# Optimization experiments

Hardware: AMD Instinct MI355X
Metric: run time of the kernel (lower is better)

Reference implementation:

```python
import jax, jax.numpy as jnp
import numpy as np

NUM_EMBEDDINGS = 1024
EMBEDDING_DIM = 256
COMMITMENT_COST = 0.25


def setup_inputs() -> dict:
    key = jax.random.key(0)
    k1, k2 = jax.random.split(key)
    inputs = jax.random.normal(k1, (64, 256, 32, 32), dtype=jnp.float32)
    # nn.Embedding weight init: uniform(-1/K, 1/K)
    embedding = jax.random.uniform(
        k2, (NUM_EMBEDDINGS, EMBEDDING_DIM), dtype=jnp.float32,
        minval=-1.0 / NUM_EMBEDDINGS, maxval=1.0 / NUM_EMBEDDINGS)
    return {"inputs": inputs, "embedding": embedding}


def reference(inputs, embedding):
    # NCHW -> NHWC, flatten to [N, D]
    x = jnp.transpose(inputs, (0, 2, 3, 1))  # [B,H,W,D]
    input_shape = x.shape
    flat = x.reshape(-1, EMBEDDING_DIM)  # [N, D]

    # squared euclidean distances to all codebook entries: [N, K]
    distances = (jnp.sum(flat ** 2, axis=1, keepdims=True)
                 + jnp.sum(embedding ** 2, axis=1)
                 - 2.0 * flat @ embedding.T)
    idx = jnp.argmin(distances, axis=1)  # [N]

    # one-hot encodings (returned output); quantization via gather is
    # mathematically identical to encodings @ embedding
    encodings = jax.nn.one_hot(idx, NUM_EMBEDDINGS, dtype=embedding.dtype)  # [N,K]
    quantized_flat = embedding[idx]  # [N, D]
    quantized = quantized_flat.reshape(input_shape)  # [B,H,W,D]

    e_latent_loss = jnp.mean((jax.lax.stop_gradient(quantized) - x) ** 2)
    q_latent_loss = jnp.mean((quantized - jax.lax.stop_gradient(x)) ** 2)
    loss = q_latent_loss + COMMITMENT_COST * e_latent_loss

    # straight-through estimator
    quantized_st = x + jax.lax.stop_gradient(quantized - x)

    avg_probs = jnp.mean(encodings, axis=0)  # [K]
    perplexity = jnp.exp(-jnp.sum(avg_probs * jnp.log(avg_probs + 1e-10)))

    quantized_out = jnp.transpose(quantized_st, (0, 3, 1, 2))  # NHWC -> NCHW
    return (loss, quantized_out, perplexity, encodings, quantized_flat)
```

## Files before the change

### kernel.cpp

```cpp
#include <hip/hip_runtime.h>
#include <hip/hip_bf16.h>
#include <math.h>

#define NB    64
#define D     256
#define K     1024
#define HW    1024
#define NTOT  65536
#define MARGIN 1e-5f

#define OUT_QOUT   1
#define OUT_PERP   16777217
#define OUT_ENC    16777218
#define OUT_QFLAT  83886082


typedef __attribute__((ext_vector_type(8))) short bf16x8;
typedef __attribute__((ext_vector_type(4))) float f32x4;

__global__ void enorm_kernel(const float* __restrict__ emb, float* __restrict__ enorm) {
    int k = blockIdx.x * 256 + threadIdx.x;
    const float4* row = (const float4*)(emb + (size_t)k * D);
    float s = 0.f;
    #pragma unroll
    for (int q = 0; q < D / 4; q++) {
        float4 v = row[q];
        s += v.x * v.x + v.y * v.y + v.z * v.z + v.w * v.w;
    }
    enorm[k] = s;
}

__global__ void esplit_kernel(const float* __restrict__ emb, ushort* __restrict__ efrag) {
    const int ntg = blockIdx.x;
    const int t = threadIdx.x;
    __shared__ float sEm[16 * 260];

    {
        const int row = t >> 4, seg = t & 15;
        const float4* src = (const float4*)(emb + (size_t)(ntg * 16 + row) * D + seg * 16);
        float4* dst = (float4*)(sEm + row * 260 + seg * 16);
        #pragma unroll
        for (int q = 0; q < 4; q++) dst[q] = src[q];
    }
    __syncthreads();

    const int w = t >> 6, lane = t & 63;
    for (int fb = w; fb < 16; fb += 4) {
        const int h = fb >> 3, dc = fb & 7;
        const float* srcp = sEm + (lane & 15) * 260 + dc * 32 + (lane >> 4) * 8;
        ushort o[8];
        #pragma unroll
        for (int j = 0; j < 8; j++) {
            float x = srcp[j];
            __hip_bfloat16 hb = __float2bfloat16(x);
            if (h == 0) { o[j] = *(ushort*)&hb; }
            else {
                float hf = __bfloat162float(hb);
                __hip_bfloat16 lb = __float2bfloat16(x - hf);
                o[j] = *(ushort*)&lb;
            }
        }
        ushort* dst = efrag + ((size_t)(h * 64 + ntg) * 8 + dc) * 512 + lane * 8;
        *(int4*)dst = *(int4*)o;
    }
}

__global__ void __attribute__((amdgpu_flat_work_group_size(256, 256), amdgpu_waves_per_eu(2, 2)))
score_mfma_kernel(
    const float* __restrict__ in, const ushort* __restrict__ efrag,
    const float* __restrict__ enorm, int* __restrict__ idx,
    int* __restrict__ rcount, int* __restrict__ rlist)
{
    __shared__ ushort sA[16384];

    const int t = threadIdx.x;
    const int n0 = blockIdx.x * 32;
    const int b = n0 >> 10, p0 = n0 & 1023;
    const int w = t >> 6, lane = t & 63;

    {
        #pragma unroll
        for (int i = 0; i < 4; i++) {
            const int fb = w * 4 + i;
            const int mt = fb >> 3, dc = fb & 7;
            const int m  = mt * 16 + (lane & 15);
            const int d0 = dc * 32 + (lane >> 4) * 8;
            const float* src = in + (size_t)b * (D * HW) + (size_t)d0 * HW + p0 + m;
            ushort oh[8], ol[8];
            #pragma unroll
            for (int j = 0; j < 8; j++) {
                const float x = src[(size_t)j * HW];
                __hip_bfloat16 hb = __float2bfloat16(x);
                const float hf = __bfloat162float(hb);
                __hip_bfloat16 lb = __float2bfloat16(x - hf);
                oh[j] = *(ushort*)&hb;
                ol[j] = *(ushort*)&lb;
            }
            ushort* dh = sA + ((0 * 2 + mt) * 8 + dc) * 512 + lane * 8;
            ushort* dl = sA + ((1 * 2 + mt) * 8 + dc) * 512 + lane * 8;
            *(int4*)dh = *(int4*)oh;
            *(int4*)dl = *(int4*)ol;
        }
    }
    __syncthreads();

    float rm1[8], rm2[8]; int ri[8];
    #pragma unroll
    for (int q = 0; q < 8; q++) { rm1[q] = 3.4e38f; rm2[q] = 3.4e38f; ri[q] = 0; }

    const ushort* efragLo = efrag + 262144;

    for (int kp = 0; kp < 4; kp++) {
        f32x4 acc[2][4];
        #pragma unroll
        for (int mt = 0; mt < 2; mt++)
            #pragma unroll
            for (int c = 0; c < 4; c++) acc[mt][c] = (f32x4){0.f, 0.f, 0.f, 0.f};

        bf16x8 Bh[4][2], Bl[4][2];
        #pragma unroll
        for (int s = 0; s < 3; s++) {
            const int dc = s >> 1, cp = s & 1;
            const int ntg0 = kp * 16 + w * 4 + cp * 2;
            const size_t o0 = ((size_t)(ntg0 * 8 + dc)) * 512 + lane * 8;
            Bh[s][0] = *(const bf16x8*)(efrag + o0);
            Bl[s][0] = *(const bf16x8*)(efragLo + o0);
            Bh[s][1] = *(const bf16x8*)(efrag + o0 + 8 * 512);
            Bl[s][1] = *(const bf16x8*)(efragLo + o0 + 8 * 512);
        }

        bf16x8 ah[2], al[2];
        #pragma unroll
        for (int s = 0; s < 16; s++) {
            const int dc = s >> 1, cp = s & 1;
            if (s + 3 < 16) {
                const int s2 = s + 3, dc2 = s2 >> 1, cp2 = s2 & 1, bs2 = s2 & 3;
                const int ntg0 = kp * 16 + w * 4 + cp2 * 2;
                const size_t o0 = ((size_t)(ntg0 * 8 + dc2)) * 512 + lane * 8;
                Bh[bs2][0] = *(const bf16x8*)(efrag + o0);
                Bl[bs2][0] = *(const bf16x8*)(efragLo + o0);
                Bh[bs2][1] = *(const bf16x8*)(efrag + o0 + 8 * 512);
                Bl[bs2][1] = *(const bf16x8*)(efragLo + o0 + 8 * 512);
            }
            if (cp == 0) {
                #pragma unroll
                for (int mt = 0; mt < 2; mt++) {
                    ah[mt] = *(const bf16x8*)(sA + ((0 * 2 + mt) * 8 + dc) * 512 + lane * 8);
                    al[mt] = *(const bf16x8*)(sA + ((1 * 2 + mt) * 8 + dc) * 512 + lane * 8);
                }
            }
            const int bs = s & 3;
            #pragma unroll
            for (int mt = 0; mt < 2; mt++) {
                #pragma unroll
                for (int cc = 0; cc < 2; cc++) {
                    const int c = cp * 2 + cc;
                    acc[mt][c] = __builtin_amdgcn_mfma_f32_16x16x32_bf16(al[mt], Bh[bs][cc], acc[mt][c], 0, 0, 0);
                    acc[mt][c] = __builtin_amdgcn_mfma_f32_16x16x32_bf16(ah[mt], Bh[bs][cc], acc[mt][c], 0, 0, 0);
                    acc[mt][c] = __builtin_amdgcn_mfma_f32_16x16x32_bf16(ah[mt], Bl[bs][cc], acc[mt][c], 0, 0, 0);
                }
            }
        }

        #pragma unroll
        for (int c = 0; c < 4; c++) {
            const int kcc = kp * 256 + (w * 4 + c) * 16 + (lane & 15);
            const float envc = enorm[kcc];
            #pragma unroll
            for (int mt = 0; mt < 2; mt++)
                #pragma unroll
                for (int r = 0; r < 4; r++) {
                    const int q = mt * 4 + r;
                    const float s = envc - 2.0f * acc[mt][c][r];
                    if (s < rm1[q]) { rm2[q] = rm1[q]; rm1[q] = s; ri[q] = kcc; }
                    else if (s < rm2[q]) rm2[q] = s;
                }
        }
    }

    float f1 = 3.4e38f, f2 = 3.4e38f; int fi = 0;
    #pragma unroll
    for (int q = 0; q < 8; q++) {
        float m1 = rm1[q], m2 = rm2[q]; int i1 = ri[q];
        #pragma unroll
        for (int mask = 1; mask <= 8; mask <<= 1) {
            float o1 = __shfl_xor(m1, mask, 64);
            int   oi = __shfl_xor(i1, mask, 64);
            float o2 = __shfl_xor(m2, mask, 64);
            float n2 = fminf(fminf(m2, o2), fmaxf(m1, o1));
            if (o1 < m1 || (o1 == m1 && oi < i1)) { m1 = o1; i1 = oi; }
            m2 = n2;
        }
        if ((lane & 15) == q) { f1 = m1; f2 = m2; fi = i1; }
    }

    __syncthreads();
    float* sM1 = (float*)sA;
    float* sM2 = sM1 + 128;
    int*   sI  = (int*)(sM2 + 128);
    if ((lane & 15) < 8) {
        const int q = lane & 15;
        const int row = (q >> 2) * 16 + (lane >> 4) * 4 + (q & 3);
        sM1[w * 32 + row] = f1;
        sM2[w * 32 + row] = f2;
        sI [w * 32 + row] = fi;
    }
    __syncthreads();
    if (t < 32) {
        float b1 = sM1[t], b2 = sM2[t]; int bi = sI[t];
        #pragma unroll
        for (int ww = 1; ww < 4; ww++) {
            float a1 = sM1[ww * 32 + t], a2 = sM2[ww * 32 + t]; int ai = sI[ww * 32 + t];
            float n2 = fminf(fminf(b2, a2), fmaxf(b1, a1));
            if (a1 < b1 || (a1 == b1 && ai < bi)) { b1 = a1; bi = ai; }
            b2 = n2;
        }
        const int n = n0 + t;
        idx[n] = bi;
        if (b2 - b1 < MARGIN) {
            int pos = atomicAdd(rcount, 1);
            rlist[pos] = n;
        }
    }
}

__global__ void rescue_kernel(const float* __restrict__ in, const float* __restrict__ emb,
                              const int* __restrict__ rcount, const int* __restrict__ rlist,
                              int* __restrict__ idx)
{
    const int wid = blockIdx.x * 4 + (threadIdx.x >> 6);
    const int lane = threadIdx.x & 63;
    const int count = *rcount;
    for (int li = wid; li < count; li += 512 * 4) {
        const int n = rlist[li];
        const int b = n >> 10, p = n & 1023;
        const float* f = in + (size_t)b * (D * HW) + p;
        float fr[4];
        #pragma unroll
        for (int q = 0; q < 4; q++) fr[q] = f[(size_t)(lane + q * 64) * HW];
        double bm = 1e300; int bk = 0;
        #pragma unroll 1
        for (int kk = 0; kk < 16; kk++) {
            const int k = lane + kk * 64;
            const float4* er4 = (const float4*)(emb + (size_t)k * D);
            double sc[4];
            #pragma unroll
            for (int q = 0; q < 4; q++) sc[q] = 0.0;
            #pragma unroll
            for (int q = 0; q < 4; q++) {
                #pragma unroll
                for (int f4 = 0; f4 < 16; f4++) {
                    const float4 ev4 = er4[q * 16 + f4];
                    #pragma unroll
                    for (int e = 0; e < 4; e++) {
                        const int dl = f4 * 4 + e;
                        const double fv = (double)__shfl(fr[q], dl, 64);
                        const double ev = (double)((const float*)&ev4)[e];
                        sc[q] += ev * (ev - 2.0 * fv);
                    }
                }
            }
            const double s = (sc[0] + sc[1]) + (sc[2] + sc[3]);
            if (s < bm) { bm = s; bk = k; }
        }
        #pragma unroll
        for (int off = 32; off >= 1; off >>= 1) {
            double om = __shfl_xor(bm, off, 64);
            int    ok = __shfl_xor(bk, off, 64);
            if (om < bm || (om == bm && ok < bk)) { bm = om; bk = ok; }
        }
        if (lane == 0) idx[n] = bk;
    }
}

__global__ __launch_bounds__(256) void outputs_kernel(
    const float* __restrict__ in, const float* __restrict__ emb,
    const int* __restrict__ idx, float* __restrict__ out,
    double* __restrict__ lossPartial, int* __restrict__ hist)
{
    __shared__ int skv[32];
    __shared__ float sQ[32 * 260];
    __shared__ double sred[4];

    const int t = threadIdx.x;
    const int n0 = blockIdx.x * 32;
    const int b = n0 >> 10, p0 = n0 & 1023;

    if (t < 32) skv[t] = idx[n0 + t];
    __syncthreads();

    {
        const int r = t >> 3, c0 = (t & 7) * 32;
        const int kv = skv[r];
        const float4* src = (const float4*)(emb + (size_t)kv * D + c0);
        float4* dstL = (float4*)(sQ + r * 260 + c0);
        float4* dstG = (float4*)(out + OUT_QFLAT + (size_t)(n0 + r) * D + c0);
        #pragma unroll
        for (int g = 0; g < 8; g++) {
            float4 v = src[g];
            dstL[g] = v;
            dstG[g] = v;
        }
    }
    {
        float* encBase = out + OUT_ENC + (size_t)n0 * K;
        const int c0 = t * 4;
        #pragma unroll 4
        for (int r = 0; r < 32; r++) {
            const int kv = skv[r];
            float4 v = make_float4(0.f, 0.f, 0.f, 0.f);
            if (kv >= c0 && kv < c0 + 4) ((float*)&v)[kv - c0] = 1.0f;
            *(float4*)(encBase + (size_t)r * K + c0) = v;
        }
    }
    if (t < 32) atomicAdd(&hist[skv[t]], 1);
    __syncthreads();

    const int p = t & 31, dg = t >> 5;
    double acc = 0.0;
    const size_t obase = (size_t)b * (D * HW) + p0 + p;
    #pragma unroll
    for (int dd = 0; dd < 32; dd++) {
        const int d = dg * 32 + dd;
        const float q = sQ[p * 260 + d];
        const float x = in[obase + (size_t)d * HW];
        out[OUT_QOUT + obase + (size_t)d * HW] = q;
        const float df = q - x;
        acc += (double)(df * df);
    }
    #pragma unroll
    for (int off = 32; off >= 1; off >>= 1) acc += __shfl_xor(acc, off, 64);
    if ((t & 63) == 0) sred[t >> 6] = acc;
    __syncthreads();
    if (t == 0) lossPartial[blockIdx.x] = sred[0] + sred[1] + sred[2] + sred[3];
}

__global__ void finalize_kernel(const int* __restrict__ hist, const double* __restrict__ lossPartial,
                                float* __restrict__ out)
{
    const int t = threadIdx.x;
    double s = 0.0;
    #pragma unroll
    for (int q = 0; q < 4; q++) {
        const int c = hist[t + q * 256];
        const double p = (double)c / (double)NTOT;
        s += p * log(p + 1e-10);
    }
    double l = 0.0;
    #pragma unroll
    for (int q = 0; q < 8; q++) l += lossPartial[t + q * 256];
    #pragma unroll
    for (int off = 32; off >= 1; off >>= 1) {
        s += __shfl_xor(s, off, 64);
        l += __shfl_xor(l, off, 64);
    }
    __shared__ double sr[4], lr[4];
    if ((t & 63) == 0) { sr[t >> 6] = s; lr[t >> 6] = l; }
    __syncthreads();
    if (t == 0) {
        out[0] = (float)(1.25 * (lr[0] + lr[1] + lr[2] + lr[3]) / (double)(NTOT * (size_t)D));
        out[OUT_PERP] = (float)exp(-(sr[0] + sr[1] + sr[2] + sr[3]));
    }
}

extern "C" void kernel_launch(void* const* d_in, const int* in_sizes, int n_in,
                              void* d_out, int out_size, void* d_ws, size_t ws_size,
                              hipStream_t stream)
{
    const float* in  = (const float*)d_in[0];
    const float* emb = (const float*)d_in[1];
    float* out = (float*)d_out;
    char* ws = (char*)d_ws;

    int*    rcount      = (int*)(ws + 0);
    int*    hist        = (int*)(ws + 16);
    float*  enorm       = (float*)(ws + 4112);
    int*    idx         = (int*)(ws + 8208);
    int*    rlist       = (int*)(ws + 270352);
    double* lossPartial = (double*)(ws + 532496);
    ushort* efrag       = (ushort*)(ws + 548880);

    hipMemsetAsync(ws, 0, 8208, stream);

    enorm_kernel<<<K / 256, 256, 0, stream>>>(emb, enorm);
    esplit_kernel<<<K / 16, 256, 0, stream>>>(emb, efrag);
    score_mfma_kernel<<<NTOT / 32, 256, 0, stream>>>(in, efrag, enorm, idx, rcount, rlist);
    rescue_kernel<<<512, 256, 0, stream>>>(in, emb, rcount, rlist, idx);
    outputs_kernel<<<NTOT / 32, 256, 0, stream>>>(in, emb, idx, out, lossPartial, hist);
    finalize_kernel<<<1, 256, 0, stream>>>(hist, lossPartial, out);
}
```

Baseline: 912.6 us.

## Fuse output writes and loss into score kernel, patch rescued rows afterwards

Moves the quantized gather, one-hot encoding writes, NCHW output writes, histogram and loss partials into the scoring kernel. The loss is now computed from the bf16 hi/lo split already held in shared memory, so the input is not read a second time. The rescue kernel patches any row whose index changes by fixing its encoding, histogram, outputs and a loss delta. The embedding-norm kernel is folded into the split kernel. This removes one full pass over the input and one kernel launch, at the cost of extra shared memory and register pressure in the score kernel, which may lower its occupancy.

```diff
diff --git a/kernel.cpp b/kernel.cpp
--- a/kernel.cpp
+++ b/kernel.cpp
@@ -18,19 +18,12 @@
 typedef __attribute__((ext_vector_type(8))) short bf16x8;
 typedef __attribute__((ext_vector_type(4))) float f32x4;
 
-__global__ void enorm_kernel(const float* __restrict__ emb, float* __restrict__ enorm) {
-    int k = blockIdx.x * 256 + threadIdx.x;
-    const float4* row = (const float4*)(emb + (size_t)k * D);
-    float s = 0.f;
-    #pragma unroll
-    for (int q = 0; q < D / 4; q++) {
-        float4 v = row[q];
-        s += v.x * v.x + v.y * v.y + v.z * v.z + v.w * v.w;
-    }
-    enorm[k] = s;
-}
-
-__global__ void esplit_kernel(const float* __restrict__ emb, ushort* __restrict__ efrag) {
+static __device__ __forceinline__ float bf2f(ushort u) {
+    return __uint_as_float(((unsigned int)u) << 16);
+}
+
+__global__ void esplit_kernel(const float* __restrict__ emb, ushort* __restrict__ efrag,
+                              float* __restrict__ enorm) {
     const int ntg = blockIdx.x;
     const int t = threadIdx.x;
     __shared__ float sEm[16 * 260];
@@ -43,6 +36,19 @@
         for (int q = 0; q < 4; q++) dst[q] = src[q];
     }
     __syncthreads();
+
+    {
+        const int row = t >> 4, seg = t & 15;
+        float s = 0.f;
+        #pragma unroll
+        for (int u = 0; u < 16; u++) {
+            const float v = sEm[row * 260 + seg * 16 + u];
+            s += v * v;
+        }
+        #pragma unroll
+        for (int mask = 1; mask <= 8; mask <<= 1) s += __shfl_xor(s, mask, 64);
+        if (seg == 0) enorm[ntg * 16 + row] = s;
+    }
 
     const int w = t >> 6, lane = t & 63;
     for (int fb = w; fb < 16; fb += 4) {
@@ -66,12 +72,18 @@
 }
 
 __global__ void __attribute__((amdgpu_flat_work_group_size(256, 256), amdgpu_waves_per_eu(2, 2)))
-score_mfma_kernel(
+score_fused_kernel(
     const float* __restrict__ in, const ushort* __restrict__ efrag,
-    const float* __restrict__ enorm, int* __restrict__ idx,
-    int* __restrict__ rcount, int* __restrict__ rlist)
+    const float* __restrict__ enorm, const float* __restrict__ emb,
+    int* __restrict__ idx, int* __restrict__ rcount, int* __restrict__ rlist,
+    float* __restrict__ out, double* __restrict__ lossPartial, int* __restrict__ hist)
 {
     __shared__ ushort sA[16384];
+    __shared__ float  sQ[32 * 260];
+    __shared__ float  sM1[128], sM2[128];
+    __shared__ int    sIm[128];
+    __shared__ int    skv[32];
+    __shared__ double sred[4];
 
     const int t = threadIdx.x;
     const int n0 = blockIdx.x * 32;
@@ -194,39 +206,105 @@
         if ((lane & 15) == q) { f1 = m1; f2 = m2; fi = i1; }
     }
 
-    __syncthreads();
-    float* sM1 = (float*)sA;
-    float* sM2 = sM1 + 128;
-    int*   sI  = (int*)(sM2 + 128);
     if ((lane & 15) < 8) {
         const int q = lane & 15;
         const int row = (q >> 2) * 16 + (lane >> 4) * 4 + (q & 3);
         sM1[w * 32 + row] = f1;
         sM2[w * 32 + row] = f2;
-        sI [w * 32 + row] = fi;
+        sIm[w * 32 + row] = fi;
     }
     __syncthreads();
     if (t < 32) {
-        float b1 = sM1[t], b2 = sM2[t]; int bi = sI[t];
+        float b1 = sM1[t], b2 = sM2[t]; int bi = sIm[t];
         #pragma unroll
         for (int ww = 1; ww < 4; ww++) {
-            float a1 = sM1[ww * 32 + t], a2 = sM2[ww * 32 + t]; int ai = sI[ww * 32 + t];
+            float a1 = sM1[ww * 32 + t], a2 = sM2[ww * 32 + t]; int ai = sIm[ww * 32 + t];
             float n2 = fminf(fminf(b2, a2), fmaxf(b1, a1));
             if (a1 < b1 || (a1 == b1 && ai < bi)) { b1 = a1; bi = ai; }
             b2 = n2;
         }
         const int n = n0 + t;
         idx[n] = bi;
+        skv[t] = bi;
         if (b2 - b1 < MARGIN) {
             int pos = atomicAdd(rcount, 1);
             rlist[pos] = n;
         }
+        atomicAdd(&hist[bi], 1);
+    }
+    __syncthreads();
+
+    {
+        const int r = t >> 3, c0 = (t & 7) * 32;
+        const int kv = skv[r];
+        const float4* src = (const float4*)(emb + (size_t)kv * D + c0);
+        float4* dstL = (float4*)(sQ + r * 260 + c0);
+        float4* dstG = (float4*)(out + OUT_QFLAT + (size_t)(n0 + r) * D + c0);
+        #pragma unroll
+        for (int g = 0; g < 8; g++) {
+            float4 v = src[g];
+            dstL[g] = v;
+            dstG[g] = v;
+        }
+    }
+    {
+        float* encBase = out + OUT_ENC + (size_t)n0 * K;
+        const int c0 = t * 4;
+        #pragma unroll 4
+        for (int r = 0; r < 32; r++) {
+            const int kv = skv[r];
+            float4 v = make_float4(0.f, 0.f, 0.f, 0.f);
+            if (kv >= c0 && kv < c0 + 4) ((float*)&v)[kv - c0] = 1.0f;
+            *(float4*)(encBase + (size_t)r * K + c0) = v;
+        }
+    }
+    __syncthreads();
+
+    {
+        const int p = t & 31, dg = t >> 5;
+        const size_t obase = (size_t)b * (D * HW) + p0 + p;
+        #pragma unroll
+        for (int dd = 0; dd < 32; dd++) {
+            const int d = dg * 32 + dd;
+            out[OUT_QOUT + obase + (size_t)d * HW] = sQ[p * 260 + d];
+        }
+    }
+
+    {
+        double lacc = 0.0;
+        #pragma unroll
+        for (int i = 0; i < 4; i++) {
+            const int fb = w * 4 + i;
+            const int mt = fb >> 3, dc = fb & 7;
+            const int m  = mt * 16 + (lane & 15);
+            const int d0 = dc * 32 + (lane >> 4) * 8;
+            const int kv = skv[m];
+            bf16x8 hv = *(const bf16x8*)(sA + ((0 * 2 + mt) * 8 + dc) * 512 + lane * 8);
+            bf16x8 lv = *(const bf16x8*)(sA + ((1 * 2 + mt) * 8 + dc) * 512 + lane * 8);
+            const float4 q0 = *(const float4*)(emb + (size_t)kv * D + d0);
+            const float4 q1 = *(const float4*)(emb + (size_t)kv * D + d0 + 4);
+            float accf = 0.f;
+            #pragma unroll
+            for (int j = 0; j < 8; j++) {
+                const float x = bf2f((ushort)hv[j]) + bf2f((ushort)lv[j]);
+                const float qv = (j < 4) ? ((const float*)&q0)[j] : ((const float*)&q1)[j - 4];
+                const float df = qv - x;
+                accf += df * df;
+            }
+            lacc += (double)accf;
+        }
+        #pragma unroll
+        for (int off = 32; off >= 1; off >>= 1) lacc += __shfl_xor(lacc, off, 64);
+        if ((t & 63) == 0) sred[w] = lacc;
+        __syncthreads();
+        if (t == 0) lossPartial[blockIdx.x] = sred[0] + sred[1] + sred[2] + sred[3];
     }
 }
 
 __global__ void rescue_kernel(const float* __restrict__ in, const float* __restrict__ emb,
                               const int* __restrict__ rcount, const int* __restrict__ rlist,
-                              int* __restrict__ idx)
+                              int* __restrict__ idx, float* __restrict__ out,
+                              int* __restrict__ hist, double* __restrict__ lossDelta)
 {
     const int wid = blockIdx.x * 4 + (threadIdx.x >> 6);
     const int lane = threadIdx.x & 63;
@@ -269,74 +347,41 @@
             int    ok = __shfl_xor(bk, off, 64);
             if (om < bm || (om == bm && ok < bk)) { bm = om; bk = ok; }
         }
-        if (lane == 0) idx[n] = bk;
-    }
-}
-
-__global__ __launch_bounds__(256) void outputs_kernel(
-    const float* __restrict__ in, const float* __restrict__ emb,
-    const int* __restrict__ idx, float* __restrict__ out,
-    double* __restrict__ lossPartial, int* __restrict__ hist)
-{
-    __shared__ int skv[32];
-    __shared__ float sQ[32 * 260];
-    __shared__ double sred[4];
-
-    const int t = threadIdx.x;
-    const int n0 = blockIdx.x * 32;
-    const int b = n0 >> 10, p0 = n0 & 1023;
-
-    if (t < 32) skv[t] = idx[n0 + t];
-    __syncthreads();
-
-    {
-        const int r = t >> 3, c0 = (t & 7) * 32;
-        const int kv = skv[r];
-        const float4* src = (const float4*)(emb + (size_t)kv * D + c0);
-        float4* dstL = (float4*)(sQ + r * 260 + c0);
-        float4* dstG = (float4*)(out + OUT_QFLAT + (size_t)(n0 + r) * D + c0);
-        #pragma unroll
-        for (int g = 0; g < 8; g++) {
-            float4 v = src[g];
-            dstL[g] = v;
-            dstG[g] = v;
-        }
-    }
-    {
-        float* encBase = out + OUT_ENC + (size_t)n0 * K;
-        const int c0 = t * 4;
-        #pragma unroll 4
-        for (int r = 0; r < 32; r++) {
-            const int kv = skv[r];
-            float4 v = make_float4(0.f, 0.f, 0.f, 0.f);
-            if (kv >= c0 && kv < c0 + 4) ((float*)&v)[kv - c0] = 1.0f;
-            *(float4*)(encBase + (size_t)r * K + c0) = v;
-        }
-    }
-    if (t < 32) atomicAdd(&hist[skv[t]], 1);
-    __syncthreads();
-
-    const int p = t & 31, dg = t >> 5;
-    double acc = 0.0;
-    const size_t obase = (size_t)b * (D * HW) + p0 + p;
-    #pragma unroll
-    for (int dd = 0; dd < 32; dd++) {
-        const int d = dg * 32 + dd;
-        const float q = sQ[p * 260 + d];
-        const float x = in[obase + (size_t)d * HW];
-        out[OUT_QOUT + obase + (size_t)d * HW] = q;
-        const float df = q - x;
-        acc += (double)(df * df);
-    }
-    #pragma unroll
-    for (int off = 32; off >= 1; off >>= 1) acc += __shfl_xor(acc, off, 64);
-    if ((t & 63) == 0) sred[t >> 6] = acc;
-    __syncthreads();
-    if (t == 0) lossPartial[blockIdx.x] = sred[0] + sred[1] + sred[2] + sred[3];
+
+        const int old = idx[n];
+        if (bk != old) {
+            const float* eb = emb + (size_t)bk * D;
+            const float* eo = emb + (size_t)old * D;
+            if (lane == 0) {
+                idx[n] = bk;
+                out[OUT_ENC + (size_t)n * K + old] = 0.f;
+                out[OUT_ENC + (size_t)n * K + bk]  = 1.f;
+                atomicAdd(&hist[old], -1);
+                atomicAdd(&hist[bk], 1);
+            }
+            *(float4*)(out + OUT_QFLAT + (size_t)n * D + lane * 4) =
+                *(const float4*)(eb + lane * 4);
+            double dl = 0.0;
+            #pragma unroll
+            for (int q = 0; q < 4; q++) {
+                const int d = lane + q * 64;
+                const float x  = fr[q];
+                const float qn = eb[d];
+                const float qo = eo[d];
+                out[OUT_QOUT + (size_t)b * (D * HW) + (size_t)d * HW + p] = qn;
+                const double dn = (double)qn - (double)x;
+                const double dO = (double)qo - (double)x;
+                dl += dn * dn - dO * dO;
+            }
+            #pragma unroll
+            for (int off = 32; off >= 1; off >>= 1) dl += __shfl_xor(dl, off, 64);
+            if (lane == 0) atomicAdd(lossDelta, dl);
+        }
+    }
 }
 
 __global__ void finalize_kernel(const int* __restrict__ hist, const double* __restrict__ lossPartial,
-                                float* __restrict__ out)
+                                const double* __restrict__ lossDelta, float* __restrict__ out)
 {
     const int t = threadIdx.x;
     double s = 0.0;
@@ -358,7 +403,8 @@
     if ((t & 63) == 0) { sr[t >> 6] = s; lr[t >> 6] = l; }
     __syncthreads();
     if (t == 0) {
-        out[0] = (float)(1.25 * (lr[0] + lr[1] + lr[2] + lr[3]) / (double)(NTOT * (size_t)D));
+        const double ltot = lr[0] + lr[1] + lr[2] + lr[3] + *lossDelta;
+        out[0] = (float)(1.25 * ltot / (double)(NTOT * (size_t)D));
         out[OUT_PERP] = (float)exp(-(sr[0] + sr[1] + sr[2] + sr[3]));
     }
 }
@@ -373,6 +419,7 @@
     char* ws = (char*)d_ws;
 
     int*    rcount      = (int*)(ws + 0);
+    double* lossDelta   = (double*)(ws + 8);
     int*    hist        = (int*)(ws + 16);
     float*  enorm       = (float*)(ws + 4112);
     int*    idx         = (int*)(ws + 8208);
@@ -382,10 +429,10 @@
 
     hipMemsetAsync(ws, 0, 8208, stream);
 
-    enorm_kernel<<<K / 256, 256, 0, stream>>>(emb, enorm);
-    esplit_kernel<<<K / 16, 256, 0, stream>>>(emb, efrag);
-    score_mfma_kernel<<<NTOT / 32, 256, 0, stream>>>(in, efrag, enorm, idx, rcount, rlist);
-    rescue_kernel<<<512, 256, 0, stream>>>(in, emb, rcount, rlist, idx);
-    outputs_kernel<<<NTOT / 32, 256, 0, stream>>>(in, emb, idx, out, lossPartial, hist);
-    finalize_kernel<<<1, 256, 0, stream>>>(hist, lossPartial, out);
-}
+    esplit_kernel<<<K / 16, 256, 0, stream>>>(emb, efrag, enorm);
+    score_fused_kernel<<<NTOT / 32, 256, 0, stream>>>(in, efrag, enorm, emb,
+                                                      idx, rcount, rlist,
+                                                      out, lossPartial, hist);
+    rescue_kernel<<<512, 256, 0, stream>>>(in, emb, rcount, rlist, idx, out, hist, lossDelta);
+    finalize_kernel<<<1, 256, 0, stream>>>(hist, lossPartial, lossDelta, out);
+}
```

New measurement: 817.0 us. -10.5%, faster.
